# Kernel tuning notes

Hardware: AMD Instinct MI355X
Metric: run time of the kernel (lower is better)

## Reference

```python
import jax, jax.numpy as jnp
import numpy as np

D_MODEL = 1024
N_HEADS = 16
HEAD_DIM = D_MODEL // N_HEADS


def setup_inputs() -> dict:
    key = jax.random.key(0)
    ks = jax.random.split(key, 5)
    x = jax.random.normal(ks[0], (4, 2048, D_MODEL), dtype=jnp.float32)
    # qkv Linear: weight [3*d_model, d_model], bias [3*d_model]
    w_qkv = jax.random.normal(ks[1], (3 * D_MODEL, D_MODEL), dtype=jnp.float32) / np.sqrt(D_MODEL)
    b_qkv = jnp.zeros((3 * D_MODEL,), dtype=jnp.float32)
    w_out = jax.random.normal(ks[2], (D_MODEL, D_MODEL), dtype=jnp.float32) / np.sqrt(D_MODEL)
    b_out = jnp.zeros((D_MODEL,), dtype=jnp.float32)
    return {"x": x, "w_qkv": w_qkv, "b_qkv": b_qkv, "w_out": w_out, "b_out": b_out}


def reference(x, w_qkv, b_qkv, w_out, b_out):
    B, T, C = x.shape
    H, Dh = N_HEADS, HEAD_DIM
    qkv = x @ w_qkv.T + b_qkv                      # [B,T,3C]
    qkv = qkv.reshape(B, T, 3, H, Dh)
    q = jnp.transpose(qkv[:, :, 0], (0, 2, 1, 3))  # [B,H,T,Dh]
    k = jnp.transpose(qkv[:, :, 1], (0, 2, 1, 3))
    v = jnpp_transpose = jnp.transpose(qkv[:, :, 2], (0, 2, 1, 3))
    scale = 1.0 / np.sqrt(Dh).astype(np.float32)
    att = jnp.einsum('bhqd,bhkd->bhqk', q, k) * scale
    causal = jnp.tril(jnp.ones((T, T), dtype=bool))
    att = jnp.where(causal[None, None], att, -jnp.inf)
    att = jax.nn.softmax(att, axis=-1)
    head_out = jnp.einsum('bhqk,bhkd->bhqd', att, v)  # [B,H,T,Dh]
    out = jnp.transpose(head_out, (0, 2, 1, 3)).reshape(B, T, C)
    return out @ w_out.T + b_out
```

## Files before the change

### kernel.cpp

```cpp
#include <hip/hip_runtime.h>
#include <hip/hip_bf16.h>


#define D_MODEL 1024
#define N_HEADS 16
#define HEAD_DIM 64
#define SEQ 2048
#define BATCH 4

typedef __attribute__((ext_vector_type(8))) short bf16x8;
typedef __attribute__((ext_vector_type(4))) float f32x4;
typedef unsigned int uint;

__device__ __forceinline__ short f2bf(float f) {
    union { float f; uint i; } c; c.f = f;
    uint x = c.i;
    x += 0x7fffu + ((x >> 16) & 1u);
    return (short)(x >> 16);
}
__device__ __forceinline__ uint pack2(float a, float b) {
    return (uint)(unsigned short)f2bf(a) | ((uint)(unsigned short)f2bf(b) << 16);
}
__device__ __forceinline__ uint asu(float f) { union { float f; uint i; } c; c.f = f; return c.i; }
__device__ __forceinline__ uint packtr(float lo, float hi) {
    return __builtin_amdgcn_perm(asu(hi), asu(lo), 0x07060302u);
}

__device__ __forceinline__ void glds16(const void* g, void* l) {
    __builtin_amdgcn_global_load_lds(
        (const __attribute__((address_space(1))) uint*)g,
        (__attribute__((address_space(3))) uint*)l, 16, 0, 0);
}

__global__ __launch_bounds__(256) void cvt3_bf16(const float* __restrict__ s0,
                                                 const float* __restrict__ s1,
                                                 const float* __restrict__ s2,
                                                 short* __restrict__ dst,
                                                 int n0, int n01) {
    int i = blockIdx.x * 256 + threadIdx.x;
    const float* src;
    int off;
    if (i < n0)       { src = s0; off = i; }
    else if (i < n01) { src = s1; off = i - n0; }
    else              { src = s2; off = i - n01; }
    float4 f = *(const float4*)(src + (size_t)off * 4);
    uint2 o; o.x = pack2(f.x, f.y); o.y = pack2(f.z, f.w);
    *(uint2*)(dst + (size_t)i * 4) = o;
}

template <int MODE>
__global__ __launch_bounds__(256, 2) void gemm_bt(
    const short* __restrict__ A, const short* __restrict__ B,
    const float* __restrict__ bias, float* __restrict__ Cp,
    int M, int N, int K,
    short* __restrict__ qp, short* __restrict__ kp, short* __restrict__ vp)
{
    __shared__ short As[2][128][32];
    __shared__ short Bs[2][128][32];
    const int tid = threadIdx.x;
    const int wave = tid >> 6, lane = tid & 63;
    const int quad = lane >> 4, l16 = lane & 15;
    const int wm = (wave >> 1) * 64, wn = (wave & 1) * 64;
    const int rowBase = blockIdx.y * 128;
    const int colBase = blockIdx.x * 128;

    const short* gA = A + (size_t)(rowBase + wave * 32 + (lane >> 2)) * K + (lane & 3) * 8;
    const short* gB = B + (size_t)(colBase + wave * 32 + (lane >> 2)) * K + (lane & 3) * 8;

    f32x4 acc[4][4] = {};
    const int NT = K / 32;

#define GSTAGE(buf, k0)                                                \
    {                                                                  \
        glds16(gA + (k0), &As[buf][wave * 32][0]);                     \
        glds16(gA + (size_t)16 * K + (k0), &As[buf][wave * 32 + 16][0]); \
        glds16(gB + (k0), &Bs[buf][wave * 32][0]);                     \
        glds16(gB + (size_t)16 * K + (k0), &Bs[buf][wave * 32 + 16][0]); \
    }

    GSTAGE(0, 0)

    for (int t = 0; t < NT; ++t) {
        const int cur = t & 1;
        __builtin_amdgcn_s_barrier();
        __builtin_amdgcn_sched_barrier(0);
        if (t + 1 < NT) GSTAGE(cur ^ 1, (t + 1) * 32)
        __builtin_amdgcn_sched_barrier(0);
        if (t + 1 < NT) asm volatile("s_waitcnt vmcnt(8)" ::: "memory");
        else            asm volatile("s_waitcnt vmcnt(0)" ::: "memory");
        __builtin_amdgcn_sched_barrier(0);

        bf16x8 af[4], bfr[4];
#pragma unroll
        for (int i = 0; i < 4; ++i)
            af[i] = *(const bf16x8*)&As[cur][wm + i * 16 + l16][quad * 8];
#pragma unroll
        for (int j = 0; j < 4; ++j)
            bfr[j] = *(const bf16x8*)&Bs[cur][wn + j * 16 + l16][quad * 8];
        __builtin_amdgcn_s_setprio(1);
#pragma unroll
        for (int i = 0; i < 4; ++i)
#pragma unroll
            for (int j = 0; j < 4; ++j)
                acc[i][j] = __builtin_amdgcn_mfma_f32_16x16x32_bf16(af[i], bfr[j], acc[i][j], 0, 0, 0);
        __builtin_amdgcn_s_setprio(0);
    }
#undef GSTAGE

#pragma unroll
    for (int i = 0; i < 4; ++i) {
#pragma unroll
        for (int j = 0; j < 4; ++j) {
#pragma unroll
            for (int r = 0; r < 4; ++r) {
                int row = rowBase + wm + i * 16 + quad * 4 + r;
                int col = colBase + wn + j * 16 + l16;
                float v = acc[i][j][r] + bias[col];
                if (MODE == 0) {
                    Cp[(size_t)row * N + col] = v;
                } else {
                    int which = col >> 10;
                    int h = (col >> 6) & 15;
                    int d = col & 63;
                    int b = row >> 11;
                    int t2 = row & 2047;
                    short* dst = (which == 0) ? qp : (which == 1) ? kp : vp;
                    dst[((((size_t)b * N_HEADS + h) * SEQ) + t2) * HEAD_DIM + d] = f2bf(v);
                }
            }
        }
    }
}

__global__ __launch_bounds__(256, 2) void attn_fwd(
    const short* __restrict__ Q, const short* __restrict__ K,
    const short* __restrict__ V, short* __restrict__ O)
{
    __shared__ short Ks[64][72];
    __shared__ short Vt[64][72];
    __shared__ short Ps[128][72];
    const int tid = threadIdx.x;
    const int wave = tid >> 6, lane = tid & 63;
    const int quad = lane >> 4, l16 = lane & 15;
    const int bh = blockIdx.x;
    const int b = bh >> 4, h = bh & 15;
    const int y = blockIdx.y, y0 = y & 3, g = y >> 2;
    const int qt = (g == 0) ? 15 - y0 : (g == 1) ? 8 + y0 : (g == 2) ? 7 - y0 : y0;
    const int qbase = qt * 128;
    const short* Qh = Q + (size_t)bh * SEQ * HEAD_DIM;
    const short* Kh = K + (size_t)bh * SEQ * HEAD_DIM;
    const short* Vh = V + (size_t)bh * SEQ * HEAD_DIM;

    const float C1 = 0.125f * 1.44269504f;
    const float C2 = 14.4269504f;

    bf16x8 onesf;
#pragma unroll
    for (int e = 0; e < 8; ++e) onesf[e] = (short)0x3F80;

    bf16x8 qf[2][2];
#pragma unroll
    for (int m = 0; m < 2; ++m)
#pragma unroll
        for (int st = 0; st < 2; ++st)
            qf[m][st] = *(const bf16x8*)(Qh + (size_t)(qbase + wave * 32 + m * 16 + l16) * HEAD_DIM + st * 32 + quad * 8);

    f32x4 o[2][4] = {};
    f32x4 osum[2] = {};

    const int subw = qbase + wave * 32;
    const int subS = __builtin_amdgcn_readfirstlane(subw);

    const int kr = tid >> 2, kc = (tid & 3) * 16;
    const int vk = (tid & 31) * 2, vd = (tid >> 5) * 8;

    const int ntiles = 2 * qt + 2;
    int4 kv0 = *(const int4*)(Kh + (size_t)kr * HEAD_DIM + kc);
    int4 kv1 = *(const int4*)(Kh + (size_t)kr * HEAD_DIM + kc + 8);
    int4 vv0 = *(const int4*)(Vh + (size_t)vk * HEAD_DIM + vd);
    int4 vv1 = *(const int4*)(Vh + (size_t)(vk + 1) * HEAD_DIM + vd);

    for (int j = 0; j < ntiles; ++j) {
        const int kb = j * 64;
        __syncthreads();
        *(int4*)&Ks[kr][kc] = kv0;
        *(int4*)&Ks[kr][kc + 8] = kv1;
        {
            const uint* pa = (const uint*)&vv0;
            const uint* pb = (const uint*)&vv1;
#pragma unroll
            for (int e = 0; e < 4; ++e) {
                uint lo = __builtin_amdgcn_perm(pb[e], pa[e], 0x05040100u);
                uint hi = __builtin_amdgcn_perm(pb[e], pa[e], 0x07060302u);
                *(uint*)&Vt[vd + 2 * e][vk] = lo;
                *(uint*)&Vt[vd + 2 * e + 1][vk] = hi;
            }
        }
        __syncthreads();

        if (j + 1 < ntiles) {
            const int kbn = kb + 64;
            kv0 = *(const int4*)(Kh + (size_t)(kbn + kr) * HEAD_DIM + kc);
            kv1 = *(const int4*)(Kh + (size_t)(kbn + kr) * HEAD_DIM + kc + 8);
            vv0 = *(const int4*)(Vh + (size_t)(kbn + vk) * HEAD_DIM + vd);
            vv1 = *(const int4*)(Vh + (size_t)(kbn + vk + 1) * HEAD_DIM + vd);
        }

        if (kb > subS + 31) continue;

        {
            const int prowb = wave * 32 + l16;
#pragma unroll
            for (int kt = 0; kt < 4; ++kt) {
                const int kbkt = kb + kt * 16;
                bf16x8 kf0, kf1;
                if (kbkt <= subS + 31) {
                    kf0 = *(const bf16x8*)&Ks[kt * 16 + l16][quad * 8];
                    kf1 = *(const bf16x8*)&Ks[kt * 16 + l16][32 + quad * 8];
                }
#pragma unroll
                for (int m = 0; m < 2; ++m) {
                    const int sub = subS + m * 16;
                    uint2 u;
                    if (kbkt > sub + 15) {
                        u.x = 0u; u.y = 0u;
                    } else {
                        f32x4 tt = {0.f, 0.f, 0.f, 0.f};
                        tt = __builtin_amdgcn_mfma_f32_16x16x32_bf16(kf0, qf[m][0], tt, 0, 0, 0);
                        tt = __builtin_amdgcn_mfma_f32_16x16x32_bf16(kf1, qf[m][1], tt, 0, 0, 0);
                        float p[4];
                        if (kbkt + 15 <= sub) {
#pragma unroll
                            for (int r = 0; r < 4; ++r)
                                p[r] = __builtin_exp2f(__builtin_fmaf(tt[r], C1, -C2));
                        } else {
                            const int qrow = sub + l16;
#pragma unroll
                            for (int r = 0; r < 4; ++r) {
                                float a = __builtin_fmaf(tt[r], C1, -C2);
                                if (kbkt + quad * 4 + r > qrow) a = -1e30f;
                                p[r] = __builtin_exp2f(a);
                            }
                        }
                        u.x = packtr(p[0], p[1]); u.y = packtr(p[2], p[3]);
                    }
                    *(uint2*)&Ps[prowb + m * 16][kt * 16 + quad * 4] = u;
                }
            }
        }
#pragma unroll
        for (int st = 0; st < 2; ++st) {
            if (st == 1 && kb + 32 > subS + 31) break;
            bf16x8 pf0 = *(const bf16x8*)&Ps[wave * 32 + l16][st * 32 + quad * 8];
            bf16x8 pf1 = *(const bf16x8*)&Ps[wave * 32 + 16 + l16][st * 32 + quad * 8];
            __builtin_amdgcn_s_setprio(1);
            osum[0] = __builtin_amdgcn_mfma_f32_16x16x32_bf16(pf0, onesf, osum[0], 0, 0, 0);
            osum[1] = __builtin_amdgcn_mfma_f32_16x16x32_bf16(pf1, onesf, osum[1], 0, 0, 0);
#pragma unroll
            for (int dt = 0; dt < 4; ++dt) {
                bf16x8 vf = *(const bf16x8*)&Vt[dt * 16 + l16][st * 32 + quad * 8];
                o[0][dt] = __builtin_amdgcn_mfma_f32_16x16x32_bf16(pf0, vf, o[0][dt], 0, 0, 0);
                o[1][dt] = __builtin_amdgcn_mfma_f32_16x16x32_bf16(pf1, vf, o[1][dt], 0, 0, 0);
            }
            __builtin_amdgcn_s_setprio(0);
        }
    }

#pragma unroll
    for (int m = 0; m < 2; ++m) {
#pragma unroll
        for (int r = 0; r < 4; ++r) {
            float inv = 1.f / osum[m][r];
            int t = qbase + wave * 32 + m * 16 + quad * 4 + r;
            size_t base = ((size_t)b * SEQ + t) * D_MODEL + h * HEAD_DIM;
#pragma unroll
            for (int dt = 0; dt < 4; ++dt)
                O[base + dt * 16 + l16] = f2bf(o[m][dt][r] * inv);
        }
    }
}

extern "C" void kernel_launch(void* const* d_in, const int* in_sizes, int n_in,
                              void* d_out, int out_size, void* d_ws, size_t ws_size,
                              hipStream_t stream)
{
    const float* x     = (const float*)d_in[0];
    const float* w_qkv = (const float*)d_in[1];
    const float* b_qkv = (const float*)d_in[2];
    const float* w_out = (const float*)d_in[3];
    const float* b_out = (const float*)d_in[4];
    float* out = (float*)d_out;

    const int NX = BATCH * SEQ * D_MODEL;
    const int NWQ = 3 * D_MODEL * D_MODEL;
    const int NWO = D_MODEL * D_MODEL;
    const size_t HE = (size_t)BATCH * N_HEADS * SEQ * HEAD_DIM;

    short* xb    = (short*)d_ws;
    short* wqkvb = xb + NX;
    short* woutb = wqkvb + NWQ;
    short* qp    = woutb + NWO;
    short* kp    = qp + HE;
    short* vp    = kp + HE;
    short* ho    = xb;

    const int M = BATCH * SEQ;

    cvt3_bf16<<<(NX + NWQ + NWO) / 1024, 256, 0, stream>>>(
        x, w_qkv, w_out, xb, NX / 4, (NX + NWQ) / 4);

    gemm_bt<1><<<dim3(3 * D_MODEL / 128, M / 128), 256, 0, stream>>>(
        xb, wqkvb, b_qkv, nullptr, M, 3 * D_MODEL, D_MODEL, qp, kp, vp);

    attn_fwd<<<dim3(BATCH * N_HEADS, SEQ / 128), 256, 0, stream>>>(qp, kp, vp, ho);

    gemm_bt<0><<<dim3(D_MODEL / 128, M / 128), 256, 0, stream>>>(
        ho, woutb, b_out, out, M, D_MODEL, D_MODEL, nullptr, nullptr, nullptr);
}
```

Before: 252.7 us.

## Switch attention to 32x32x16 MFMA with register-resident P via permlane32 swap

Rewrites the attention kernel to use 32x32x16 bf16 MFMA tiles instead of 16x16x32. The softmax probabilities stay in registers and are rearranged into the A-operand layout with v_permlane32_swap, which removes the Ps shared-memory buffer and its write/read round trip. Dropping that buffer shrinks LDS use, and the launch bound is raised to 4 blocks per CU for more occupancy. The risk is higher register pressure from the 16-wide accumulators under the tighter occupancy bound, plus a layout change that must keep the masking correct.

```diff
diff --git a/kernel.cpp b/kernel.cpp
--- a/kernel.cpp
+++ b/kernel.cpp
@@ -10,6 +10,7 @@
 
 typedef __attribute__((ext_vector_type(8))) short bf16x8;
 typedef __attribute__((ext_vector_type(4))) float f32x4;
+typedef __attribute__((ext_vector_type(16))) float f32x16;
 typedef unsigned int uint;
 
 __device__ __forceinline__ short f2bf(float f) {
@@ -132,16 +133,15 @@
     }
 }
 
-__global__ __launch_bounds__(256, 2) void attn_fwd(
+__global__ __launch_bounds__(256, 4) void attn_fwd(
     const short* __restrict__ Q, const short* __restrict__ K,
     const short* __restrict__ V, short* __restrict__ O)
 {
     __shared__ short Ks[64][72];
     __shared__ short Vt[64][72];
-    __shared__ short Ps[128][72];
     const int tid = threadIdx.x;
     const int wave = tid >> 6, lane = tid & 63;
-    const int quad = lane >> 4, l16 = lane & 15;
+    const int l31 = lane & 31, hi = lane >> 5;
     const int bh = blockIdx.x;
     const int b = bh >> 4, h = bh & 15;
     const int y = blockIdx.y, y0 = y & 3, g = y >> 2;
@@ -158,18 +158,17 @@
 #pragma unroll
     for (int e = 0; e < 8; ++e) onesf[e] = (short)0x3F80;
 
-    bf16x8 qf[2][2];
-#pragma unroll
-    for (int m = 0; m < 2; ++m)
-#pragma unroll
-        for (int st = 0; st < 2; ++st)
-            qf[m][st] = *(const bf16x8*)(Qh + (size_t)(qbase + wave * 32 + m * 16 + l16) * HEAD_DIM + st * 32 + quad * 8);
-
-    f32x4 o[2][4] = {};
-    f32x4 osum[2] = {};
+    bf16x8 qf[4];
+#pragma unroll
+    for (int ks = 0; ks < 4; ++ks)
+        qf[ks] = *(const bf16x8*)(Qh + (size_t)(qbase + wave * 32 + l31) * HEAD_DIM + ks * 16 + hi * 8);
+
+    f32x16 o[2] = {};
+    f32x16 osum = {};
 
     const int subw = qbase + wave * 32;
     const int subS = __builtin_amdgcn_readfirstlane(subw);
+    const int qrow = subS + l31;
 
     const int kr = tid >> 2, kc = (tid & 3) * 16;
     const int vk = (tid & 31) * 2, vd = (tid >> 5) * 8;
@@ -186,14 +185,14 @@
         *(int4*)&Ks[kr][kc] = kv0;
         *(int4*)&Ks[kr][kc + 8] = kv1;
         {
-            const uint* pa = (const uint*)&vv0;
-            const uint* pb = (const uint*)&vv1;
+            const uint* pa_ = (const uint*)&vv0;
+            const uint* pb_ = (const uint*)&vv1;
 #pragma unroll
             for (int e = 0; e < 4; ++e) {
-                uint lo = __builtin_amdgcn_perm(pb[e], pa[e], 0x05040100u);
-                uint hi = __builtin_amdgcn_perm(pb[e], pa[e], 0x07060302u);
+                uint lo = __builtin_amdgcn_perm(pb_[e], pa_[e], 0x05040100u);
+                uint hi2 = __builtin_amdgcn_perm(pb_[e], pa_[e], 0x07060302u);
                 *(uint*)&Vt[vd + 2 * e][vk] = lo;
-                *(uint*)&Vt[vd + 2 * e + 1][vk] = hi;
+                *(uint*)&Vt[vd + 2 * e + 1][vk] = hi2;
             }
         }
         __syncthreads();
@@ -208,75 +207,69 @@
 
         if (kb > subS + 31) continue;
 
-        {
-            const int prowb = wave * 32 + l16;
-#pragma unroll
-            for (int kt = 0; kt < 4; ++kt) {
-                const int kbkt = kb + kt * 16;
-                bf16x8 kf0, kf1;
-                if (kbkt <= subS + 31) {
-                    kf0 = *(const bf16x8*)&Ks[kt * 16 + l16][quad * 8];
-                    kf1 = *(const bf16x8*)&Ks[kt * 16 + l16][32 + quad * 8];
+        bf16x8 pa[4];
+#pragma unroll
+        for (int kt = 0; kt < 2; ++kt) {
+            const int base = kb + kt * 32;
+            if (base > subS + 31) continue;
+            f32x16 s = {};
+#pragma unroll
+            for (int ks = 0; ks < 4; ++ks) {
+                bf16x8 kf = *(const bf16x8*)&Ks[kt * 32 + l31][ks * 16 + hi * 8];
+                s = __builtin_amdgcn_mfma_f32_32x32x16_bf16(kf, qf[ks], s, 0, 0, 0);
+            }
+            uint c[8];
+            if (base + 31 <= subS) {
+#pragma unroll
+                for (int pr = 0; pr < 8; ++pr) {
+                    float plo = __builtin_exp2f(__builtin_fmaf(s[2 * pr], C1, -C2));
+                    float phi = __builtin_exp2f(__builtin_fmaf(s[2 * pr + 1], C1, -C2));
+                    c[pr] = packtr(plo, phi);
                 }
-#pragma unroll
-                for (int m = 0; m < 2; ++m) {
-                    const int sub = subS + m * 16;
-                    uint2 u;
-                    if (kbkt > sub + 15) {
-                        u.x = 0u; u.y = 0u;
-                    } else {
-                        f32x4 tt = {0.f, 0.f, 0.f, 0.f};
-                        tt = __builtin_amdgcn_mfma_f32_16x16x32_bf16(kf0, qf[m][0], tt, 0, 0, 0);
-                        tt = __builtin_amdgcn_mfma_f32_16x16x32_bf16(kf1, qf[m][1], tt, 0, 0, 0);
-                        float p[4];
-                        if (kbkt + 15 <= sub) {
-#pragma unroll
-                            for (int r = 0; r < 4; ++r)
-                                p[r] = __builtin_exp2f(__builtin_fmaf(tt[r], C1, -C2));
-                        } else {
-                            const int qrow = sub + l16;
-#pragma unroll
-                            for (int r = 0; r < 4; ++r) {
-                                float a = __builtin_fmaf(tt[r], C1, -C2);
-                                if (kbkt + quad * 4 + r > qrow) a = -1e30f;
-                                p[r] = __builtin_exp2f(a);
-                            }
-                        }
-                        u.x = packtr(p[0], p[1]); u.y = packtr(p[2], p[3]);
-                    }
-                    *(uint2*)&Ps[prowb + m * 16][kt * 16 + quad * 4] = u;
+            } else {
+                const int khi = base + 4 * hi;
+                float p[16];
+#pragma unroll
+                for (int r = 0; r < 16; ++r) {
+                    float a = __builtin_fmaf(s[r], C1, -C2);
+                    if (khi + (r & 3) + 8 * (r >> 2) > qrow) a = -1e30f;
+                    p[r] = __builtin_exp2f(a);
                 }
-            }
-        }
-#pragma unroll
-        for (int st = 0; st < 2; ++st) {
-            if (st == 1 && kb + 32 > subS + 31) break;
-            bf16x8 pf0 = *(const bf16x8*)&Ps[wave * 32 + l16][st * 32 + quad * 8];
-            bf16x8 pf1 = *(const bf16x8*)&Ps[wave * 32 + 16 + l16][st * 32 + quad * 8];
+#pragma unroll
+                for (int pr = 0; pr < 8; ++pr) c[pr] = packtr(p[2 * pr], p[2 * pr + 1]);
+            }
+            asm volatile("v_permlane32_swap_b32 %0, %1" : "+v"(c[0]), "+v"(c[2]));
+            asm volatile("v_permlane32_swap_b32 %0, %1" : "+v"(c[1]), "+v"(c[3]));
+            asm volatile("v_permlane32_swap_b32 %0, %1" : "+v"(c[4]), "+v"(c[6]));
+            asm volatile("v_permlane32_swap_b32 %0, %1" : "+v"(c[5]), "+v"(c[7]));
+            uint4 u0; u0.x = c[0]; u0.y = c[1]; u0.z = c[2]; u0.w = c[3];
+            uint4 u1; u1.x = c[4]; u1.y = c[5]; u1.z = c[6]; u1.w = c[7];
+            pa[2 * kt] = *(bf16x8*)&u0;
+            pa[2 * kt + 1] = *(bf16x8*)&u1;
+        }
+
+#pragma unroll
+        for (int ks = 0; ks < 4; ++ks) {
+            if (kb + ks * 16 > subS + 31) break;
             __builtin_amdgcn_s_setprio(1);
-            osum[0] = __builtin_amdgcn_mfma_f32_16x16x32_bf16(pf0, onesf, osum[0], 0, 0, 0);
-            osum[1] = __builtin_amdgcn_mfma_f32_16x16x32_bf16(pf1, onesf, osum[1], 0, 0, 0);
-#pragma unroll
-            for (int dt = 0; dt < 4; ++dt) {
-                bf16x8 vf = *(const bf16x8*)&Vt[dt * 16 + l16][st * 32 + quad * 8];
-                o[0][dt] = __builtin_amdgcn_mfma_f32_16x16x32_bf16(pf0, vf, o[0][dt], 0, 0, 0);
-                o[1][dt] = __builtin_amdgcn_mfma_f32_16x16x32_bf16(pf1, vf, o[1][dt], 0, 0, 0);
+            osum = __builtin_amdgcn_mfma_f32_32x32x16_bf16(pa[ks], onesf, osum, 0, 0, 0);
+#pragma unroll
+            for (int dt = 0; dt < 2; ++dt) {
+                bf16x8 vf = *(const bf16x8*)&Vt[dt * 32 + l31][ks * 16 + hi * 8];
+                o[dt] = __builtin_amdgcn_mfma_f32_32x32x16_bf16(pa[ks], vf, o[dt], 0, 0, 0);
             }
             __builtin_amdgcn_s_setprio(0);
         }
     }
 
 #pragma unroll
-    for (int m = 0; m < 2; ++m) {
-#pragma unroll
-        for (int r = 0; r < 4; ++r) {
-            float inv = 1.f / osum[m][r];
-            int t = qbase + wave * 32 + m * 16 + quad * 4 + r;
-            size_t base = ((size_t)b * SEQ + t) * D_MODEL + h * HEAD_DIM;
-#pragma unroll
-            for (int dt = 0; dt < 4; ++dt)
-                O[base + dt * 16 + l16] = f2bf(o[m][dt][r] * inv);
-        }
+    for (int r = 0; r < 16; ++r) {
+        float inv = 1.f / osum[r];
+        int t = qbase + wave * 32 + (r & 3) + 8 * (r >> 2) + 4 * hi;
+        size_t base = ((size_t)b * SEQ + t) * D_MODEL + h * HEAD_DIM;
+#pragma unroll
+        for (int dt = 0; dt < 2; ++dt)
+            O[base + dt * 32 + l31] = f2bf(o[dt][r] * inv);
     }
 }
 
```

Measured after the change: 280.1 us. +10.9%, slower.
